# Performance work log

Measured on AMD Instinct MI355X. Metric: run time of the kernel, lower is better.

Reference implementation:

```python
import jax, jax.numpy as jnp
from jax import lax
import numpy as np

IN_SIZE, H_SIZE, OUT_SIZE, SEAS = 48, 128, 48, 24
DILATIONS = (1, 2, 4, 8)  # cells 0-1 = DRNN group 0, cells 2-3 = DRNN group 1


def setup_inputs() -> dict:
    key = jax.random.key(0)
    ks = jax.random.split(key, 16)
    B, T = 256, 512
    inp = {
        'train': jax.random.uniform(ks[0], (B, T), jnp.float32, 0.5, 1.5),
        'val': jax.random.uniform(ks[1], (B, OUT_SIZE), jnp.float32, 0.5, 1.5),
        'test': jax.random.uniform(ks[2], (B, OUT_SIZE), jnp.float32, 0.5, 1.5),
        'init_lev_sm': jnp.array([0.5], jnp.float32),
        'init_seas_sm': jnp.array([0.5], jnp.float32),
        'init_seasonalities': jnp.full((SEAS,), 0.5, jnp.float32),
    }
    cin = [IN_SIZE, H_SIZE, H_SIZE, H_SIZE]
    k = 3
    for i in range(4):
        inp[f'w_ih{i}'] = jax.random.normal(ks[k], (4 * H_SIZE, cin[i]), jnp.float32) * 0.05; k += 1
        inp[f'w_hh{i}'] = jax.random.normal(ks[k], (4 * H_SIZE, H_SIZE), jnp.float32) * 0.05; k += 1
        inp[f'b_ih{i}'] = jnp.zeros((4 * H_SIZE,), jnp.float32)
        inp[f'b_hh{i}'] = jnp.zeros((4 * H_SIZE,), jnp.float32)
    inp['nl_w'] = jax.random.normal(ks[k], (H_SIZE, H_SIZE), jnp.float32) * 0.05; k += 1
    inp['nl_b'] = jnp.zeros((H_SIZE,), jnp.float32)
    inp['sc_w'] = jax.random.normal(ks[k], (OUT_SIZE, H_SIZE), jnp.float32) * 0.05; k += 1
    inp['sc_b'] = jnp.zeros((OUT_SIZE,), jnp.float32)
    return inp


def _lstm(x, w_ih, w_hh, b_ih, b_hh):
    # x: (T, N, C) -> (T, N, H); torch LSTM gate order i, f, g, o
    n, h = x.shape[1], w_hh.shape[1]

    def step(carry, xt):
        hp, cp = carry
        g = xt @ w_ih.T + hp @ w_hh.T + (b_ih + b_hh)
        i, f, gg, o = jnp.split(g, 4, axis=-1)
        c = jax.nn.sigmoid(f) * cp + jax.nn.sigmoid(i) * jnp.tanh(gg)
        hn = jax.nn.sigmoid(o) * jnp.tanh(c)
        return (hn, c), hn

    z = jnp.zeros((n, h), x.dtype)
    _, hs = lax.scan(step, (z, z), x)
    return hs


def _dilated_lstm(x, d, w_ih, w_hh, b_ih, b_hh):
    # DRNN dilation: fold time by d into batch, run cell, unfold
    t, b, c = x.shape
    td = -(-t // d) * d
    xp = jnp.pad(x, ((0, td - t), (0, 0), (0, 0)))
    xd = xp.reshape(td // d, d, b, c).reshape(td // d, d * b, c)
    out = _lstm(xd, w_ih, w_hh, b_ih, b_hh)
    h = out.shape[-1]
    return out.reshape(td // d, d, b, h).reshape(td, b, h)[:t]


def _series_forward(data, cells, nl_w, nl_b, sc_w, sc_b):
    # ResidualDRNN: group 0 (cells 0,1), group 1 (cells 2,3) with residual add
    x = data
    for grp in range(2):
        res = x
        for ci in (2 * grp, 2 * grp + 1):
            x = _dilated_lstm(x, DILATIONS[ci], *cells[ci])
        if grp > 0:
            x = x + res
    x = jnp.tanh(x @ nl_w.T + nl_b)
    return x @ sc_w.T + sc_b


def _esrnn(train, val, init_lev_sm, init_seas_sm, init_seasonalities, cells, nl_w, nl_b, sc_w, sc_b):
    B, T = train.shape
    lev_sm = jax.nn.sigmoid(init_lev_sm[0])
    seas_sm = jax.nn.sigmoid(init_seas_sm[0])
    s0 = jnp.exp(init_seasonalities)  # (SEAS,) shared across series
    lev0 = train[:, 0] / s0[0]  # (B,)
    # rolling buffer: at step i it holds seasonalities[i .. i+SEAS-1]
    buf0 = jnp.broadcast_to(jnp.concatenate([s0[1:], s0[:1]])[:, None], (SEAS, B))

    def step(carry, x_t):
        lev_p, buf = carry
        seas_t = buf[0]
        lev_n = lev_sm * (x_t / seas_t) + (1 - lev_sm) * lev_p
        seas_n = seas_sm * (x_t / lev_n) + (1 - seas_sm) * seas_t
        return (lev_n, jnp.concatenate([buf[1:], seas_n[None]], 0)), (lev_n, seas_n)

    _, (levs_r, seas_r) = lax.scan(step, (lev0, buf0), train[:, 1:].T)
    levs = jnp.concatenate([lev0[None], levs_r], 0).T  # (B, T)
    seas_head = jnp.broadcast_to(jnp.concatenate([s0, s0[:1]])[:, None], (SEAS + 1, B))
    seas = jnp.concatenate([seas_head, seas_r], 0).T  # (B, T+SEAS)
    if OUT_SIZE > SEAS:  # seasonality extension branch
        start = seas.shape[1] - SEAS
        seas = jnp.concatenate([seas, seas[:, start:start + OUT_SIZE - SEAS]], 1)
    W = T - IN_SIZE + 1
    Wo = T - OUT_SIZE - IN_SIZE + 1
    idx_in = jnp.arange(W)[:, None] + jnp.arange(IN_SIZE)[None, :]  # (W, IN)
    win_in = (train[:, idx_in] / seas[:, idx_in] / levs[:, IN_SIZE - 1:, None]).transpose(1, 0, 2)  # (W,B,IN)
    idx_out = jnp.arange(Wo)[:, None] + IN_SIZE + jnp.arange(OUT_SIZE)[None, :]
    win_out = (train[:, idx_out] / seas[:, idx_out] / levs[:, IN_SIZE - 1:IN_SIZE - 1 + Wo, None]).transpose(1, 0, 2)
    network_pred = _series_forward(win_in[:-OUT_SIZE], cells, nl_w, nl_b, sc_w, sc_b)  # (Wo,B,OUT)
    network_act = win_out
    net_out_all = _series_forward(win_in, cells, nl_w, nl_b, sc_w, sc_b)  # (W,B,OUT)
    hold = net_out_all[-1] * seas[:, -OUT_SIZE:] * levs[:, -1:]
    hold_out_pred = hold * (hold > 0).astype(hold.dtype)
    hold_out_act = val  # testing=False path
    hold_out_act_norm = val / seas[:, -OUT_SIZE:] / levs[:, -1:]
    return network_pred, network_act, hold_out_pred, net_out_all, hold_out_act, hold_out_act_norm


def reference(train, val, test, init_lev_sm, init_seas_sm, init_seasonalities,
              w_ih0, w_hh0, b_ih0, b_hh0, w_ih1, w_hh1, b_ih1, b_hh1,
              w_ih2, w_hh2, b_ih2, b_hh2, w_ih3, w_hh3, b_ih3, b_hh3,
              nl_w, nl_b, sc_w, sc_b):
    cells = ((w_ih0, w_hh0, b_ih0, b_hh0), (w_ih1, w_hh1, b_ih1, b_hh1),
             (w_ih2, w_hh2, b_ih2, b_hh2), (w_ih3, w_hh3, b_ih3, b_hh3))
    return _esrnn(train, val, init_lev_sm, init_seas_sm, init_seasonalities,
                  cells, nl_w, nl_b, sc_w, sc_b)
```

## Files before the change

### kernel.cpp

```cpp
#include <hip/hip_runtime.h>
#include <cstdint>
#include <cstddef>

typedef _Float16 half8 __attribute__((ext_vector_type(8)));
typedef _Float16 half4 __attribute__((ext_vector_type(4)));
typedef float floatx4 __attribute__((ext_vector_type(4)));

namespace {
constexpr int kB = 256, kT = 512, kIN = 48, kOUT = 48, kSEAS = 24, kH = 128;
constexpr int kW = kT - kIN + 1;
constexpr int kWO = kT - kOUT - kIN + 1;
constexpr int kNB = kW * kB;
constexpr int kMBLK = kNB / 16;
constexpr float kLOG2E = 1.44269504088896340736f;
}

#if __has_builtin(__builtin_amdgcn_exp2f)
#define FEXP2(x) __builtin_amdgcn_exp2f(x)
#else
#define FEXP2(x) exp2f(x)
#endif
#if __has_builtin(__builtin_amdgcn_rcpf)
#define FRCP(x) __builtin_amdgcn_rcpf(x)
#else
#define FRCP(x) (1.0f / (x))
#endif

__device__ __forceinline__ float fsig(float y) { return FRCP(1.0f + FEXP2(-y)); }
__device__ __forceinline__ float ftanh(float x) { return 2.0f * fsig(2.0f * kLOG2E * x) - 1.0f; }

__global__ void k_transpose(const float* __restrict__ train, float* __restrict__ trainT) {
  int t = blockIdx.x, b = threadIdx.x;
  trainT[t * kB + b] = train[b * kT + t];
}

template <int N>
__device__ __forceinline__ void es_block(int k0, int b, float lev_sm, float omb_l,
                                         float seas_sm, float omb_s, float& lev,
                                         float (&stprev)[kSEAS],
                                         const float* __restrict__ trainT,
                                         float* __restrict__ seas, float* __restrict__ levs,
                                         float* __restrict__ ratio) {
  float x[N], q[N], lv[N];
#pragma unroll
  for (int jj = 0; jj < N; ++jj) x[jj] = trainT[(k0 + jj + 1) * kB + b];
#pragma unroll
  for (int jj = 0; jj < N; ++jj) q[jj] = x[jj] * FRCP(stprev[jj]);
#pragma unroll
  for (int jj = 0; jj < N; ++jj) {
    lev = lev_sm * q[jj] + omb_l * lev;
    lv[jj] = lev;
  }
#pragma unroll
  for (int jj = 0; jj < N; ++jj) {
    float sn = seas_sm * (x[jj] * FRCP(lv[jj])) + omb_s * stprev[jj];
    stprev[jj] = sn;
    seas[(k0 + jj + kSEAS + 1) * kB + b] = sn;
    levs[(k0 + jj + 1) * kB + b] = lv[jj];
    ratio[(k0 + jj + 1) * kB + b] = q[jj];
  }
}

__global__ void k_es(const float* __restrict__ trainT, const float* __restrict__ levp,
                     const float* __restrict__ seasp, const float* __restrict__ inits,
                     float* __restrict__ seas, float* __restrict__ levs,
                     float* __restrict__ ratio) {
  int b = threadIdx.x;
  float lev_sm = fsig(levp[0] * kLOG2E);
  float seas_sm = fsig(seasp[0] * kLOG2E);
  float omb_l = 1.0f - lev_sm, omb_s = 1.0f - seas_sm;
  float stprev[kSEAS];
  float s00 = expf(inits[0]);
#pragma unroll
  for (int s = 0; s < kSEAS; ++s) {
    float v = expf(inits[s]);
    seas[s * kB + b] = v;
    if (s >= 1) stprev[s - 1] = v;
  }
  stprev[kSEAS - 1] = s00;
  seas[kSEAS * kB + b] = s00;
  float lev = trainT[b] * FRCP(s00);
  levs[b] = lev;
  ratio[b] = lev;
#pragma unroll 1
  for (int blk = 0; blk < 21; ++blk)
    es_block<24>(blk * kSEAS, b, lev_sm, omb_l, seas_sm, omb_s, lev, stprev, trainT, seas,
                 levs, ratio);
  es_block<7>(504, b, lev_sm, omb_l, seas_sm, omb_s, lev, stprev, trainT, seas, levs,
              ratio);
  for (int j = 0; j < kOUT - kSEAS; ++j)
    seas[(kT + kSEAS + j) * kB + b] = seas[(kT + j) * kB + b];
}

__global__ void k_win_in(const float* __restrict__ ratio, const float* __restrict__ levs,
                         _Float16* __restrict__ win) {
  int w = blockIdx.x;
  int tid = threadIdx.x;
#pragma unroll
  for (int i = 0; i < 16; ++i) {
    int o = i * 256 + tid;
    int b = o >> 3;
    int j0 = (o & 7) * 8;
    half8 h;
    if (j0 < kIN) {
      float rl = FRCP(levs[(kIN - 1 + w) * kB + b]);
#pragma unroll
      for (int jj = 0; jj < 8; ++jj) {
        int j = j0 + jj;
        float v = (j < kIN) ? ratio[(w + j) * kB + b] * rl : 0.0f;
        h[jj] = (_Float16)v;
      }
    } else {
#pragma unroll
      for (int jj = 0; jj < 8; ++jj) h[jj] = (_Float16)0.0f;
    }
    *(half8*)(win + ((size_t)(w * kB + b)) * 64 + j0) = h;
  }
}

__global__ void k_win_out(const float* __restrict__ ratio, const float* __restrict__ levs,
                          float* __restrict__ out1) {
  int idx = blockIdx.x * 256 + threadIdx.x;
  if (idx >= kWO * kB * (kOUT / 4)) return;
  int row = idx / 12;
  int j0 = (idx - row * 12) * 4;
  int wo = row >> 8;
  int b = row & 255;
  float rl = FRCP(levs[(kIN - 1 + wo) * kB + b]);
  floatx4 v;
#pragma unroll
  for (int jj = 0; jj < 4; ++jj) v[jj] = ratio[(kIN + wo + j0 + jj) * kB + b] * rl;
  *(floatx4*)(out1 + (size_t)row * kOUT + j0) = v;
}

__device__ __forceinline__ void prep_bias_elem(const float* bih, const float* bhh, float* dst,
                                               int c) {
  int ct = c >> 4, n16 = c & 15, g = ct & 3, wv = ct >> 2;
  int row = g * 128 + wv * 16 + n16;
  float sc = (g == 2) ? 2.0f * kLOG2E : kLOG2E;
  dst[c] = (bih[row] + bhh[row]) * sc;
}

__device__ __forceinline__ void prep_frag_elem(const float* Wsrc, _Float16* dst, int KB, int Kreal,
                                               int srcld, int perm, int idx) {
  int jj = idx & 7;
  int lane = (idx >> 3) & 63;
  int kb = (idx >> 9) % KB;
  int ct = idx / (KB * 512);
  int n16 = lane & 15;
  int k = kb * 32 + ((lane >> 4) << 3) + jj;
  int row;
  float sc;
  if (perm) {
    int g = ct & 3, wv = ct >> 2;
    row = g * 128 + wv * 16 + n16;
    sc = (g == 2) ? 2.0f * kLOG2E : kLOG2E;
  } else {
    row = ct * 16 + n16;
    sc = 1.0f;
  }
  float v = (k < Kreal) ? Wsrc[row * srcld + k] * sc : 0.0f;
  dst[idx] = (_Float16)v;
}

struct PrepArgs {
  const float* bih[4];
  const float* bhh[4];
  float* biasp[4];
  const float* wih[4];
  _Float16* wihf[4];
  const float* whh[4];
  _Float16* whhf[4];
  const float* nlw;
  _Float16* nlf;
  const float* scw;
  _Float16* scf;
};

__global__ void k_prep_all(PrepArgs a) {
  int seg = blockIdx.y;
  int idx = blockIdx.x * 256 + threadIdx.x;
  if (seg < 4) {
    if (idx < 512) prep_bias_elem(a.bih[seg], a.bhh[seg], a.biasp[seg], idx);
  } else if (seg == 4) {
    if (idx < 32 * 2 * 512) prep_frag_elem(a.wih[0], a.wihf[0], 2, 48, 48, 1, idx);
  } else if (seg < 8) {
    int c = seg - 4;
    if (idx < 32 * 4 * 512) prep_frag_elem(a.wih[c], a.wihf[c], 4, 128, 128, 1, idx);
  } else if (seg < 12) {
    int c = seg - 8;
    if (idx < 32 * 4 * 512) prep_frag_elem(a.whh[c], a.whhf[c], 4, 128, 128, 1, idx);
  } else if (seg == 12) {
    if (idx < 8 * 4 * 512) prep_frag_elem(a.nlw, a.nlf, 4, 128, 128, 0, idx);
  } else {
    if (idx < 3 * 4 * 512) prep_frag_elem(a.scw, a.scf, 4, 128, 128, 0, idx);
  }
}

__global__ void k_zero_prog(int* prog) {
  prog[threadIdx.x] = 0;
}

template <int NT, int KB, int MODE>
__global__ __launch_bounds__(512) void k_gemm(const _Float16* __restrict__ A,
                                              const _Float16* __restrict__ A2, int Khalfs,
                                              const _Float16* __restrict__ Bfr,
                                              const float* __restrict__ bias,
                                              _Float16* __restrict__ outh,
                                              float* __restrict__ outf,
                                              float* __restrict__ outf2) {
  __shared__ _Float16 bsh[NT * KB * 512];
  int tid = threadIdx.x;
  {
    const uint4* src = (const uint4*)Bfr;
    uint4* dst = (uint4*)bsh;
    for (int i = tid; i < NT * KB * 64; i += 512) dst[i] = src[i];
  }
  __syncthreads();
  int wv = tid >> 6, lane = tid & 63;
  int mblk = blockIdx.x * 8 + wv;
  if (mblk >= kMBLK) return;
  int m = lane & 15, kq = lane >> 4;
  const _Float16* arow = A + (size_t)(mblk * 16 + m) * Khalfs + kq * 8;
  half8 af[KB];
#pragma unroll
  for (int kb = 0; kb < KB; ++kb) af[kb] = *(const half8*)(arow + kb * 32);
  if constexpr (MODE == 1) {
    const _Float16* arow2 = A2 + (size_t)(mblk * 16 + m) * Khalfs + kq * 8;
#pragma unroll
    for (int kb = 0; kb < KB; ++kb) {
      half8 a2 = *(const half8*)(arow2 + kb * 32);
      af[kb] += a2;
    }
  }
#pragma unroll
  for (int t0 = 0; t0 < NT; t0 += 2) {
    float b0 = bias[t0 * 16 + m];
    floatx4 acc0 = {b0, b0, b0, b0};
    floatx4 acc1 = {0.f, 0.f, 0.f, 0.f};
    if (t0 + 1 < NT) {
      float b1 = bias[(t0 + 1) * 16 + m];
      acc1 = (floatx4){b1, b1, b1, b1};
    }
#pragma unroll
    for (int kb = 0; kb < KB; ++kb) {
      half8 bf0 = *(const half8*)(&bsh[((t0 * KB + kb) * 64 + lane) * 8]);
      acc0 = __builtin_amdgcn_mfma_f32_16x16x32_f16(af[kb], bf0, acc0, 0, 0, 0);
      if (t0 + 1 < NT) {
        half8 bf1 = *(const half8*)(&bsh[(((t0 + 1) * KB + kb) * 64 + lane) * 8]);
        acc1 = __builtin_amdgcn_mfma_f32_16x16x32_f16(af[kb], bf1, acc1, 0, 0, 0);
      }
    }
    if constexpr (MODE == 1) {
#pragma unroll
      for (int r = 0; r < 4; ++r) {
        int row = mblk * 16 + kq * 4 + r;
        outh[(size_t)row * kH + t0 * 16 + m] = (_Float16)ftanh(acc0[r]);
        if (t0 + 1 < NT) outh[(size_t)row * kH + (t0 + 1) * 16 + m] = (_Float16)ftanh(acc1[r]);
      }
    } else {
#pragma unroll
      for (int r = 0; r < 4; ++r) {
        int row = mblk * 16 + kq * 4 + r;
        float v0 = acc0[r];
        outf[(size_t)row * kOUT + t0 * 16 + m] = v0;
        if (row < kWO * kB) outf2[(size_t)row * kOUT + t0 * 16 + m] = v0;
        if (t0 + 1 < NT) {
          float v1 = acc1[r];
          outf[(size_t)row * kOUT + (t0 + 1) * 16 + m] = v1;
          if (row < kWO * kB) outf2[(size_t)row * kOUT + (t0 + 1) * 16 + m] = v1;
        }
      }
    }
  }
}

struct FArgs {
  const _Float16* win;
  const _Float16* wihf[4];
  const _Float16* whhf[4];
  const float* biasp[4];
  _Float16* H[4];
  int* prog;
};

__device__ __forceinline__ void wait_prog(int* p, int need, int& fenced, int* obs_sh) {
  if (need <= fenced) return;
  if (threadIdx.x == 0) {
    int v;
    while ((v = __hip_atomic_load(p, __ATOMIC_RELAXED, __HIP_MEMORY_SCOPE_AGENT)) < need)
      __builtin_amdgcn_s_sleep(16);
    *obs_sh = v;
  }
  __syncthreads();
  int v = *obs_sh;
  __builtin_amdgcn_fence(__ATOMIC_ACQUIRE, "agent");
  fenced = v;
}

template <int KXB, bool POLL, bool REL>
__device__ __forceinline__ void floop(const _Float16* __restrict__ Xsrc,
                                      const _Float16* __restrict__ wihp,
                                      const _Float16* __restrict__ whhp,
                                      const float* __restrict__ bp, _Float16* __restrict__ Hout,
                                      int* progIn, int sprev, int* progOut, int d, int kd, int ib,
                                      _Float16 (*hbuf)[2048], int* obs_sh) {
  int tid = threadIdx.x;
  int wv = tid >> 6, lane = tid & 63, m = lane & 15, kq = lane >> 4;
  half8 wxf[4][KXB], whf[4][4];
#pragma unroll
  for (int g = 0; g < 4; ++g) {
#pragma unroll
    for (int kb = 0; kb < KXB; ++kb)
      wxf[g][kb] = *(const half8*)(wihp + ((((wv * 4 + g) * KXB + kb) * 64 + lane) * 8));
#pragma unroll
    for (int kb = 0; kb < 4; ++kb)
      whf[g][kb] = *(const half8*)(whhp + ((((wv * 4 + g) * 4 + kb) * 64 + lane) * 8));
  }
  float bg[4];
#pragma unroll
  for (int g = 0; g < 4; ++g) bg[g] = bp[(wv * 4 + g) * 16 + m];
  float cc[4] = {0.f, 0.f, 0.f, 0.f};
  int nsteps = (kW - kd + d - 1) / d;
  const int xstride = KXB * 32;
  int fenced = 0;
  if (POLL) wait_prog(progIn + (kd & ((1 << sprev) - 1)), (kd >> sprev) + 1, fenced, obs_sh);
  half8 hxc[KXB], hxn[KXB];
  {
    const _Float16* xrow = Xsrc + (size_t)(kd * kB + ib * 16 + m) * xstride + kq * 8;
#pragma unroll
    for (int kb = 0; kb < KXB; ++kb) hxc[kb] = *(const half8*)(xrow + kb * 32);
  }
  for (int j = 0; j < nsteps; ++j) {
    int ph = j & 1;
    int wtn = (j + 1) * d + kd;
    bool havenext = (j + 1 < nsteps);
    if (POLL && havenext)
      wait_prog(progIn + (wtn & ((1 << sprev) - 1)), (wtn >> sprev) + 1, fenced, obs_sh);
    floatx4 acc[4];
#pragma unroll
    for (int g = 0; g < 4; ++g) acc[g] = (floatx4){bg[g], bg[g], bg[g], bg[g]};
    if (havenext) {
      const _Float16* xrow = Xsrc + (size_t)(wtn * kB + ib * 16 + m) * xstride + kq * 8;
#pragma unroll
      for (int kb = 0; kb < KXB; ++kb) hxn[kb] = *(const half8*)(xrow + kb * 32);
    }
#pragma unroll
    for (int kb = 0; kb < KXB; ++kb)
#pragma unroll
      for (int g = 0; g < 4; ++g)
        acc[g] = __builtin_amdgcn_mfma_f32_16x16x32_f16(hxc[kb], wxf[g][kb], acc[g], 0, 0, 0);
    if (j > 0) {
#pragma unroll
      for (int kb = 0; kb < 4; ++kb) {
        int gran = (kb * 4 + kq) ^ m;
        half8 a = *(const half8*)(&hbuf[ph ^ 1][m * 128 + gran * 8]);
#pragma unroll
        for (int g = 0; g < 4; ++g)
          acc[g] = __builtin_amdgcn_mfma_f32_16x16x32_f16(a, whf[g][kb], acc[g], 0, 0, 0);
      }
    }
    _Float16 hv[4];
#pragma unroll
    for (int r = 0; r < 4; ++r) {
      float iv = fsig(acc[0][r]);
      float fv = fsig(acc[1][r]);
      float g2 = fsig(acc[2][r]);
      float ov = fsig(acc[3][r]);
      cc[r] = fv * cc[r] + iv * (2.0f * g2 - 1.0f);
      float tc = 2.0f * fsig(cc[r] * (2.0f * kLOG2E)) - 1.0f;
      hv[r] = (_Float16)(ov * tc);
      int brow = kq * 4 + r;
      int hu = wv * 16 + m;
      int gran = (hu >> 3) ^ brow;
      hbuf[ph][brow * 128 + gran * 8 + (hu & 7)] = hv[r];
    }
    __syncthreads();
    {
      int hu = wv * 16 + m;
      size_t rb = (size_t)((j * d + kd) * kB + ib * 16 + kq * 4);
#pragma unroll
      for (int r = 0; r < 4; ++r) Hout[(rb + r) * kH + hu] = hv[r];
    }
    if (REL && (((j & 7) == 7) || (j + 1 == nsteps))) {
      __syncthreads();
      if (tid == 0)
        __hip_atomic_store(progOut, j + 1, __ATOMIC_RELEASE, __HIP_MEMORY_SCOPE_AGENT);
    }
#pragma unroll
    for (int kb = 0; kb < KXB; ++kb) hxc[kb] = hxn[kb];
  }
}

__global__ __launch_bounds__(512) void k_fused(FArgs a) {
  __shared__ _Float16 hbuf[2][2048];
  __shared__ int obs_sh;
  int w = blockIdx.x;
  int cell, d, kd, ib;
  if (w < 16) {
    cell = 0; d = 1; kd = 0; ib = w;
  } else if (w < 48) {
    cell = 1; d = 2; kd = (w - 16) >> 4; ib = (w - 16) & 15;
  } else if (w < 112) {
    cell = 2; d = 4; kd = (w - 48) >> 4; ib = (w - 48) & 15;
  } else {
    cell = 3; d = 8; kd = (w - 112) >> 4; ib = (w - 112) & 15;
  }
  const _Float16* Xsrc = (cell == 0) ? a.win : a.H[cell - 1];
  _Float16* Hout = a.H[cell];
  int* progOut = a.prog + (cell * 16 + ib) * 4 + kd;
  int* progIn = (cell > 0) ? a.prog + ((cell - 1) * 16 + ib) * 4 : nullptr;
  int sprev = (cell == 2) ? 1 : ((cell == 3) ? 2 : 0);
  if (cell == 0)
    floop<2, false, true>(Xsrc, a.wihf[0], a.whhf[0], a.biasp[0], Hout, nullptr, 0, progOut, d,
                          kd, ib, hbuf, &obs_sh);
  else if (cell < 3)
    floop<4, true, true>(Xsrc, a.wihf[cell], a.whhf[cell], a.biasp[cell], Hout, progIn, sprev,
                         progOut, d, kd, ib, hbuf, &obs_sh);
  else
    floop<4, true, false>(Xsrc, a.wihf[3], a.whhf[3], a.biasp[3], Hout, progIn, sprev, progOut,
                          d, kd, ib, hbuf, &obs_sh);
}

__global__ void k_tail(const float* __restrict__ out3, const float* __restrict__ val,
                       const float* __restrict__ seas, const float* __restrict__ levs,
                       float* __restrict__ out2, float* __restrict__ out4,
                       float* __restrict__ out5) {
  int idx = blockIdx.x * 256 + threadIdx.x;
  int b = idx / kOUT, j = idx % kOUT;
  float s = seas[(kT + j) * kB + b];
  float L = levs[(kT - 1) * kB + b];
  float net = out3[(size_t)(kW - 1) * kB * kOUT + idx];
  float hp = net * s * L;
  out2[idx] = hp > 0.0f ? hp : 0.0f;
  float v = val[idx];
  out4[idx] = v;
  out5[idx] = v / s / L;
}

extern "C" void kernel_launch(void* const* d_in, const int* in_sizes, int n_in, void* d_out,
                              int out_size, void* d_ws, size_t ws_size, hipStream_t stream) {
  const float* train = (const float*)d_in[0];
  const float* val = (const float*)d_in[1];
  const float* levp = (const float*)d_in[3];
  const float* seasp = (const float*)d_in[4];
  const float* inits = (const float*)d_in[5];
  const float* w_ih[4] = {(const float*)d_in[6], (const float*)d_in[10], (const float*)d_in[14],
                          (const float*)d_in[18]};
  const float* w_hh[4] = {(const float*)d_in[7], (const float*)d_in[11], (const float*)d_in[15],
                          (const float*)d_in[19]};
  const float* b_ih[4] = {(const float*)d_in[8], (const float*)d_in[12], (const float*)d_in[16],
                          (const float*)d_in[20]};
  const float* b_hh[4] = {(const float*)d_in[9], (const float*)d_in[13], (const float*)d_in[17],
                          (const float*)d_in[21]};
  const float* nl_w = (const float*)d_in[22];
  const float* nl_b = (const float*)d_in[23];
  const float* sc_w = (const float*)d_in[24];
  const float* sc_b = (const float*)d_in[25];

  char* wsb = (char*)d_ws;
  size_t off = 0;
  auto alloc = [&](size_t bytes) -> void* {
    void* p = wsb + off;
    off = (off + bytes + 255) & ~(size_t)255;
    return p;
  };
  float* trainT = (float*)alloc((size_t)kT * kB * 4);
  float* seas = (float*)alloc((size_t)560 * kB * 4);
  float* levs = (float*)alloc((size_t)kT * kB * 4);
  float* ratio = (float*)alloc((size_t)kT * kB * 4);
  _Float16* win = (_Float16*)alloc((size_t)kNB * 64 * 2);
  _Float16* Hc[4];
  for (int c = 0; c < 4; ++c) Hc[c] = (_Float16*)alloc((size_t)kNB * kH * 2);
  _Float16* U = (_Float16*)alloc((size_t)kNB * kH * 2);
  float* biasp[4];
  for (int c = 0; c < 4; ++c) biasp[c] = (float*)alloc(512 * 4);
  _Float16* wihf[4];
  wihf[0] = (_Float16*)alloc((size_t)32 * 2 * 512 * 2);
  for (int c = 1; c < 4; ++c) wihf[c] = (_Float16*)alloc((size_t)32 * 4 * 512 * 2);
  _Float16* whhf[4];
  for (int c = 0; c < 4; ++c) whhf[c] = (_Float16*)alloc((size_t)32 * 4 * 512 * 2);
  _Float16* nlf = (_Float16*)alloc((size_t)8 * 4 * 512 * 2);
  _Float16* scf = (_Float16*)alloc((size_t)3 * 4 * 512 * 2);
  int* prog = (int*)alloc(256 * 4);

  float* out0 = (float*)d_out;
  float* out1 = out0 + (size_t)kWO * kB * kOUT;
  float* out2 = out1 + (size_t)kWO * kB * kOUT;
  float* out3 = out2 + (size_t)kB * kOUT;
  float* out4 = out3 + (size_t)kW * kB * kOUT;
  float* out5 = out4 + (size_t)kB * kOUT;

  k_transpose<<<kT, kB, 0, stream>>>(train, trainT);
  k_es<<<1, kB, 0, stream>>>(trainT, levp, seasp, inits, seas, levs, ratio);
  k_win_in<<<kW, kB, 0, stream>>>(ratio, levs, win);
  k_win_out<<<(kWO * kB * 12 + 255) / 256, 256, 0, stream>>>(ratio, levs, out1);

  PrepArgs pa;
  for (int c = 0; c < 4; ++c) {
    pa.bih[c] = b_ih[c]; pa.bhh[c] = b_hh[c]; pa.biasp[c] = biasp[c];
    pa.wih[c] = w_ih[c]; pa.wihf[c] = wihf[c];
    pa.whh[c] = w_hh[c]; pa.whhf[c] = whhf[c];
  }
  pa.nlw = nl_w; pa.nlf = nlf; pa.scw = sc_w; pa.scf = scf;
  k_prep_all<<<dim3(256, 14), 256, 0, stream>>>(pa);
  k_zero_prog<<<1, 256, 0, stream>>>(prog);

  FArgs fa;
  fa.win = win;
  for (int c = 0; c < 4; ++c) {
    fa.wihf[c] = wihf[c]; fa.whhf[c] = whhf[c]; fa.biasp[c] = biasp[c]; fa.H[c] = Hc[c];
  }
  fa.prog = prog;
  void* kp[1] = {(void*)&fa};
  hipLaunchCooperativeKernel((void*)k_fused, dim3(240), dim3(512), kp, 0, stream);

  const int GG = kMBLK / 8;
  k_gemm<8, 4, 1><<<GG, 512, 0, stream>>>(Hc[3], Hc[1], 128, nlf, nl_b, U, nullptr, nullptr);
  k_gemm<3, 4, 2><<<GG, 512, 0, stream>>>(U, nullptr, 128, scf, sc_b, nullptr, out3, out0);
  k_tail<<<48, 256, 0, stream>>>(out3, val, seas, levs, out2, out4, out5);
}
```

Before: 687.8 us.

## Overlap output head with LSTM wavefront inside fused kernel and merge prep kernels

The separate nonlinear and scale GEMM kernels are folded into the cooperative kernel as 16 extra blocks. These blocks poll the progress counters of cells 3 and 1 and compute the head per timestep while the recurrence is still running. Cell 3 now publishes progress every 2 steps, which adds more release barriers to that cell. The transpose kernel is removed (k_es reads train rows directly), the two window kernels are merged into one, and progress zeroing moves into the prep kernel, which cuts the number of launches.

New measurement: 1.548 ms. +125.1%, slower.

```diff
diff --git a/kernel.cpp b/kernel.cpp
--- a/kernel.cpp
+++ b/kernel.cpp
@@ -13,6 +13,7 @@
 constexpr int kNB = kW * kB;
 constexpr int kMBLK = kNB / 16;
 constexpr float kLOG2E = 1.44269504088896340736f;
+constexpr int kWOBLK = (kWO * kB * 12 + 255) / 256;
 }
 
 #if __has_builtin(__builtin_amdgcn_exp2f)
@@ -26,24 +27,20 @@
 #define FRCP(x) (1.0f / (x))
 #endif
 
+#define LGKM_BARRIER() asm volatile("s_waitcnt lgkmcnt(0)\n\ts_barrier" ::: "memory")
+
 __device__ __forceinline__ float fsig(float y) { return FRCP(1.0f + FEXP2(-y)); }
 __device__ __forceinline__ float ftanh(float x) { return 2.0f * fsig(2.0f * kLOG2E * x) - 1.0f; }
-
-__global__ void k_transpose(const float* __restrict__ train, float* __restrict__ trainT) {
-  int t = blockIdx.x, b = threadIdx.x;
-  trainT[t * kB + b] = train[b * kT + t];
-}
 
 template <int N>
 __device__ __forceinline__ void es_block(int k0, int b, float lev_sm, float omb_l,
                                          float seas_sm, float omb_s, float& lev,
-                                         float (&stprev)[kSEAS],
-                                         const float* __restrict__ trainT,
+                                         float (&stprev)[kSEAS], const float* __restrict__ trow,
                                          float* __restrict__ seas, float* __restrict__ levs,
                                          float* __restrict__ ratio) {
   float x[N], q[N], lv[N];
 #pragma unroll
-  for (int jj = 0; jj < N; ++jj) x[jj] = trainT[(k0 + jj + 1) * kB + b];
+  for (int jj = 0; jj < N; ++jj) x[jj] = trow[k0 + jj + 1];
 #pragma unroll
   for (int jj = 0; jj < N; ++jj) q[jj] = x[jj] * FRCP(stprev[jj]);
 #pragma unroll
@@ -61,11 +58,12 @@
   }
 }
 
-__global__ void k_es(const float* __restrict__ trainT, const float* __restrict__ levp,
+__global__ void k_es(const float* __restrict__ train, const float* __restrict__ levp,
                      const float* __restrict__ seasp, const float* __restrict__ inits,
                      float* __restrict__ seas, float* __restrict__ levs,
                      float* __restrict__ ratio) {
   int b = threadIdx.x;
+  const float* trow = train + (size_t)b * kT;
   float lev_sm = fsig(levp[0] * kLOG2E);
   float seas_sm = fsig(seasp[0] * kLOG2E);
   float omb_l = 1.0f - lev_sm, omb_s = 1.0f - seas_sm;
@@ -79,58 +77,56 @@
   }
   stprev[kSEAS - 1] = s00;
   seas[kSEAS * kB + b] = s00;
-  float lev = trainT[b] * FRCP(s00);
+  float lev = trow[0] * FRCP(s00);
   levs[b] = lev;
   ratio[b] = lev;
 #pragma unroll 1
   for (int blk = 0; blk < 21; ++blk)
-    es_block<24>(blk * kSEAS, b, lev_sm, omb_l, seas_sm, omb_s, lev, stprev, trainT, seas,
-                 levs, ratio);
-  es_block<7>(504, b, lev_sm, omb_l, seas_sm, omb_s, lev, stprev, trainT, seas, levs,
-              ratio);
+    es_block<24>(blk * kSEAS, b, lev_sm, omb_l, seas_sm, omb_s, lev, stprev, trow, seas, levs,
+                 ratio);
+  es_block<7>(504, b, lev_sm, omb_l, seas_sm, omb_s, lev, stprev, trow, seas, levs, ratio);
   for (int j = 0; j < kOUT - kSEAS; ++j)
     seas[(kT + kSEAS + j) * kB + b] = seas[(kT + j) * kB + b];
 }
 
-__global__ void k_win_in(const float* __restrict__ ratio, const float* __restrict__ levs,
-                         _Float16* __restrict__ win) {
+__global__ void k_win(const float* __restrict__ ratio, const float* __restrict__ levs,
+                      _Float16* __restrict__ win, float* __restrict__ out1) {
   int w = blockIdx.x;
   int tid = threadIdx.x;
-#pragma unroll
-  for (int i = 0; i < 16; ++i) {
-    int o = i * 256 + tid;
-    int b = o >> 3;
-    int j0 = (o & 7) * 8;
-    half8 h;
-    if (j0 < kIN) {
-      float rl = FRCP(levs[(kIN - 1 + w) * kB + b]);
-#pragma unroll
-      for (int jj = 0; jj < 8; ++jj) {
-        int j = j0 + jj;
-        float v = (j < kIN) ? ratio[(w + j) * kB + b] * rl : 0.0f;
-        h[jj] = (_Float16)v;
-      }
-    } else {
-#pragma unroll
-      for (int jj = 0; jj < 8; ++jj) h[jj] = (_Float16)0.0f;
-    }
-    *(half8*)(win + ((size_t)(w * kB + b)) * 64 + j0) = h;
-  }
-}
-
-__global__ void k_win_out(const float* __restrict__ ratio, const float* __restrict__ levs,
-                          float* __restrict__ out1) {
-  int idx = blockIdx.x * 256 + threadIdx.x;
-  if (idx >= kWO * kB * (kOUT / 4)) return;
-  int row = idx / 12;
-  int j0 = (idx - row * 12) * 4;
-  int wo = row >> 8;
-  int b = row & 255;
-  float rl = FRCP(levs[(kIN - 1 + wo) * kB + b]);
-  floatx4 v;
-#pragma unroll
-  for (int jj = 0; jj < 4; ++jj) v[jj] = ratio[(kIN + wo + j0 + jj) * kB + b] * rl;
-  *(floatx4*)(out1 + (size_t)row * kOUT + j0) = v;
+  if (w < kW) {
+#pragma unroll
+    for (int i = 0; i < 16; ++i) {
+      int o = i * 256 + tid;
+      int b = o >> 3;
+      int j0 = (o & 7) * 8;
+      half8 h;
+      if (j0 < kIN) {
+        float rl = FRCP(levs[(kIN - 1 + w) * kB + b]);
+#pragma unroll
+        for (int jj = 0; jj < 8; ++jj) {
+          int j = j0 + jj;
+          float v = (j < kIN) ? ratio[(w + j) * kB + b] * rl : 0.0f;
+          h[jj] = (_Float16)v;
+        }
+      } else {
+#pragma unroll
+        for (int jj = 0; jj < 8; ++jj) h[jj] = (_Float16)0.0f;
+      }
+      *(half8*)(win + ((size_t)(w * kB + b)) * 64 + j0) = h;
+    }
+  } else {
+    int idx = (w - kW) * 256 + tid;
+    if (idx >= kWO * kB * 12) return;
+    int row = idx / 12;
+    int j0 = (idx - row * 12) * 4;
+    int wo = row >> 8;
+    int b = row & 255;
+    float rl = FRCP(levs[(kIN - 1 + wo) * kB + b]);
+    floatx4 v;
+#pragma unroll
+    for (int jj = 0; jj < 4; ++jj) v[jj] = ratio[(kIN + wo + j0 + jj) * kB + b] * rl;
+    *(floatx4*)(out1 + (size_t)row * kOUT + j0) = v;
+  }
 }
 
 __device__ __forceinline__ void prep_bias_elem(const float* bih, const float* bhh, float* dst,
@@ -175,6 +171,7 @@
   _Float16* nlf;
   const float* scw;
   _Float16* scf;
+  int* prog;
 };
 
 __global__ void k_prep_all(PrepArgs a) {
@@ -192,86 +189,10 @@
     if (idx < 32 * 4 * 512) prep_frag_elem(a.whh[c], a.whhf[c], 4, 128, 128, 1, idx);
   } else if (seg == 12) {
     if (idx < 8 * 4 * 512) prep_frag_elem(a.nlw, a.nlf, 4, 128, 128, 0, idx);
+  } else if (seg == 13) {
+    if (idx < 3 * 4 * 512) prep_frag_elem(a.scw, a.scf, 4, 128, 128, 0, idx);
   } else {
-    if (idx < 3 * 4 * 512) prep_frag_elem(a.scw, a.scf, 4, 128, 128, 0, idx);
-  }
-}
-
-__global__ void k_zero_prog(int* prog) {
-  prog[threadIdx.x] = 0;
-}
-
-template <int NT, int KB, int MODE>
-__global__ __launch_bounds__(512) void k_gemm(const _Float16* __restrict__ A,
-                                              const _Float16* __restrict__ A2, int Khalfs,
-                                              const _Float16* __restrict__ Bfr,
-                                              const float* __restrict__ bias,
-                                              _Float16* __restrict__ outh,
-                                              float* __restrict__ outf,
-                                              float* __restrict__ outf2) {
-  __shared__ _Float16 bsh[NT * KB * 512];
-  int tid = threadIdx.x;
-  {
-    const uint4* src = (const uint4*)Bfr;
-    uint4* dst = (uint4*)bsh;
-    for (int i = tid; i < NT * KB * 64; i += 512) dst[i] = src[i];
-  }
-  __syncthreads();
-  int wv = tid >> 6, lane = tid & 63;
-  int mblk = blockIdx.x * 8 + wv;
-  if (mblk >= kMBLK) return;
-  int m = lane & 15, kq = lane >> 4;
-  const _Float16* arow = A + (size_t)(mblk * 16 + m) * Khalfs + kq * 8;
-  half8 af[KB];
-#pragma unroll
-  for (int kb = 0; kb < KB; ++kb) af[kb] = *(const half8*)(arow + kb * 32);
-  if constexpr (MODE == 1) {
-    const _Float16* arow2 = A2 + (size_t)(mblk * 16 + m) * Khalfs + kq * 8;
-#pragma unroll
-    for (int kb = 0; kb < KB; ++kb) {
-      half8 a2 = *(const half8*)(arow2 + kb * 32);
-      af[kb] += a2;
-    }
-  }
-#pragma unroll
-  for (int t0 = 0; t0 < NT; t0 += 2) {
-    float b0 = bias[t0 * 16 + m];
-    floatx4 acc0 = {b0, b0, b0, b0};
-    floatx4 acc1 = {0.f, 0.f, 0.f, 0.f};
-    if (t0 + 1 < NT) {
-      float b1 = bias[(t0 + 1) * 16 + m];
-      acc1 = (floatx4){b1, b1, b1, b1};
-    }
-#pragma unroll
-    for (int kb = 0; kb < KB; ++kb) {
-      half8 bf0 = *(const half8*)(&bsh[((t0 * KB + kb) * 64 + lane) * 8]);
-      acc0 = __builtin_amdgcn_mfma_f32_16x16x32_f16(af[kb], bf0, acc0, 0, 0, 0);
-      if (t0 + 1 < NT) {
-        half8 bf1 = *(const half8*)(&bsh[(((t0 + 1) * KB + kb) * 64 + lane) * 8]);
-        acc1 = __builtin_amdgcn_mfma_f32_16x16x32_f16(af[kb], bf1, acc1, 0, 0, 0);
-      }
-    }
-    if constexpr (MODE == 1) {
-#pragma unroll
-      for (int r = 0; r < 4; ++r) {
-        int row = mblk * 16 + kq * 4 + r;
-        outh[(size_t)row * kH + t0 * 16 + m] = (_Float16)ftanh(acc0[r]);
-        if (t0 + 1 < NT) outh[(size_t)row * kH + (t0 + 1) * 16 + m] = (_Float16)ftanh(acc1[r]);
-      }
-    } else {
-#pragma unroll
-      for (int r = 0; r < 4; ++r) {
-        int row = mblk * 16 + kq * 4 + r;
-        float v0 = acc0[r];
-        outf[(size_t)row * kOUT + t0 * 16 + m] = v0;
-        if (row < kWO * kB) outf2[(size_t)row * kOUT + t0 * 16 + m] = v0;
-        if (t0 + 1 < NT) {
-          float v1 = acc1[r];
-          outf[(size_t)row * kOUT + (t0 + 1) * 16 + m] = v1;
-          if (row < kWO * kB) outf2[(size_t)row * kOUT + (t0 + 1) * 16 + m] = v1;
-        }
-      }
-    }
+    if (idx < 320) a.prog[idx] = 0;
   }
 }
 
@@ -282,6 +203,12 @@
   const float* biasp[4];
   _Float16* H[4];
   int* prog;
+  const _Float16* nlf;
+  const _Float16* scf;
+  const float* nlb;
+  const float* scb;
+  float* out3;
+  float* out0;
 };
 
 __device__ __forceinline__ void wait_prog(int* p, int need, int& fenced, int* obs_sh) {
@@ -298,7 +225,7 @@
   fenced = v;
 }
 
-template <int KXB, bool POLL, bool REL>
+template <int KXB, bool POLL, bool REL, int RELMASK>
 __device__ __forceinline__ void floop(const _Float16* __restrict__ Xsrc,
                                       const _Float16* __restrict__ wihp,
                                       const _Float16* __restrict__ whhp,
@@ -382,13 +309,98 @@
 #pragma unroll
       for (int r = 0; r < 4; ++r) Hout[(rb + r) * kH + hu] = hv[r];
     }
-    if (REL && (((j & 7) == 7) || (j + 1 == nsteps))) {
+    if (REL && (((j & RELMASK) == RELMASK) || (j + 1 == nsteps))) {
       __syncthreads();
       if (tid == 0)
         __hip_atomic_store(progOut, j + 1, __ATOMIC_RELEASE, __HIP_MEMORY_SCOPE_AGENT);
     }
 #pragma unroll
     for (int kb = 0; kb < KXB; ++kb) hxc[kb] = hxn[kb];
+  }
+}
+
+__device__ void tail_loop(const FArgs& a, int ib, _Float16 (*hbuf)[2048]) {
+  int tid = threadIdx.x;
+  int wv = tid >> 6, lane = tid & 63, m = lane & 15, kq = lane >> 4;
+  half8 nf[4], sf[4];
+  int cts = (wv < 3) ? wv : 0;
+#pragma unroll
+  for (int kb = 0; kb < 4; ++kb) {
+    nf[kb] = *(const half8*)(a.nlf + ((size_t)((wv * 4 + kb) * 64 + lane)) * 8);
+    sf[kb] = *(const half8*)(a.scf + ((size_t)((cts * 4 + kb) * 64 + lane)) * 8);
+  }
+  float nb = a.nlb[wv * 16 + m];
+  float sb = (wv < 3) ? a.scb[wv * 16 + m] : 0.0f;
+  int* prog3 = a.prog + 192 + ib * 8;
+  int* prog1 = a.prog + (16 + ib) * 4;
+  const _Float16* H3 = a.H[3];
+  const _Float16* H1 = a.H[1];
+  for (int t0 = 0; t0 < kW; t0 += 8) {
+    int tend = (t0 + 8 < kW) ? t0 + 8 : kW;
+    if (tid == 0) {
+      int need3 = (t0 >> 3) + 1;
+      for (int kd = 0; kd < 8; ++kd) {
+        if (t0 + kd >= tend) break;
+        while (__hip_atomic_load(prog3 + kd, __ATOMIC_RELAXED, __HIP_MEMORY_SCOPE_AGENT) < need3)
+          __builtin_amdgcn_s_sleep(16);
+      }
+      for (int kd = 0; kd < 2; ++kd) {
+        int tmaxk = tend - 1;
+        if ((tmaxk & 1) != kd) --tmaxk;
+        if (tmaxk < t0) continue;
+        int need1 = (tmaxk >> 1) + 1;
+        while (__hip_atomic_load(prog1 + kd, __ATOMIC_RELAXED, __HIP_MEMORY_SCOPE_AGENT) < need1)
+          __builtin_amdgcn_s_sleep(16);
+      }
+    }
+    __syncthreads();
+    __builtin_amdgcn_fence(__ATOMIC_ACQUIRE, "agent");
+#pragma unroll 1
+    for (int t = t0; t < tend; ++t) {
+      int ph = t & 1;
+      const _Float16* r3 = H3 + (size_t)(t * kB + ib * 16 + m) * kH + kq * 8;
+      const _Float16* r1 = H1 + (size_t)(t * kB + ib * 16 + m) * kH + kq * 8;
+      half8 af[4];
+#pragma unroll
+      for (int kb = 0; kb < 4; ++kb) {
+        half8 v3 = *(const half8*)(r3 + kb * 32);
+        half8 v1 = *(const half8*)(r1 + kb * 32);
+        af[kb] = v3 + v1;
+      }
+      floatx4 acc = {nb, nb, nb, nb};
+#pragma unroll
+      for (int kb = 0; kb < 4; ++kb)
+        acc = __builtin_amdgcn_mfma_f32_16x16x32_f16(af[kb], nf[kb], acc, 0, 0, 0);
+#pragma unroll
+      for (int r = 0; r < 4; ++r) {
+        _Float16 uv = (_Float16)ftanh(acc[r]);
+        int brow = kq * 4 + r;
+        int hu = wv * 16 + m;
+        int gran = (hu >> 3) ^ brow;
+        hbuf[ph][brow * 128 + gran * 8 + (hu & 7)] = uv;
+      }
+      LGKM_BARRIER();
+      if (wv < 3) {
+        half8 uf[4];
+#pragma unroll
+        for (int kb = 0; kb < 4; ++kb) {
+          int gran = (kb * 4 + kq) ^ m;
+          uf[kb] = *(const half8*)(&hbuf[ph][m * 128 + gran * 8]);
+        }
+        floatx4 a2 = {sb, sb, sb, sb};
+#pragma unroll
+        for (int kb = 0; kb < 4; ++kb)
+          a2 = __builtin_amdgcn_mfma_f32_16x16x32_f16(uf[kb], sf[kb], a2, 0, 0, 0);
+        size_t row = (size_t)t * kB + ib * 16 + kq * 4;
+        bool dup = (t < kWO);
+#pragma unroll
+        for (int r = 0; r < 4; ++r) {
+          float v = a2[r];
+          a.out3[(row + r) * kOUT + wv * 16 + m] = v;
+          if (dup) a.out0[(row + r) * kOUT + wv * 16 + m] = v;
+        }
+      }
+    }
   }
 }
 
@@ -396,6 +408,10 @@
   __shared__ _Float16 hbuf[2][2048];
   __shared__ int obs_sh;
   int w = blockIdx.x;
+  if (w >= 240) {
+    tail_loop(a, w - 240, hbuf);
+    return;
+  }
   int cell, d, kd, ib;
   if (w < 16) {
     cell = 0; d = 1; kd = 0; ib = w;
@@ -408,18 +424,18 @@
   }
   const _Float16* Xsrc = (cell == 0) ? a.win : a.H[cell - 1];
   _Float16* Hout = a.H[cell];
-  int* progOut = a.prog + (cell * 16 + ib) * 4 + kd;
+  int* progOut = (cell == 3) ? a.prog + 192 + ib * 8 + kd : a.prog + (cell * 16 + ib) * 4 + kd;
   int* progIn = (cell > 0) ? a.prog + ((cell - 1) * 16 + ib) * 4 : nullptr;
   int sprev = (cell == 2) ? 1 : ((cell == 3) ? 2 : 0);
   if (cell == 0)
-    floop<2, false, true>(Xsrc, a.wihf[0], a.whhf[0], a.biasp[0], Hout, nullptr, 0, progOut, d,
-                          kd, ib, hbuf, &obs_sh);
+    floop<2, false, true, 7>(Xsrc, a.wihf[0], a.whhf[0], a.biasp[0], Hout, nullptr, 0, progOut,
+                             d, kd, ib, hbuf, &obs_sh);
   else if (cell < 3)
-    floop<4, true, true>(Xsrc, a.wihf[cell], a.whhf[cell], a.biasp[cell], Hout, progIn, sprev,
-                         progOut, d, kd, ib, hbuf, &obs_sh);
+    floop<4, true, true, 7>(Xsrc, a.wihf[cell], a.whhf[cell], a.biasp[cell], Hout, progIn,
+                            sprev, progOut, d, kd, ib, hbuf, &obs_sh);
   else
-    floop<4, true, false>(Xsrc, a.wihf[3], a.whhf[3], a.biasp[3], Hout, progIn, sprev, progOut,
-                          d, kd, ib, hbuf, &obs_sh);
+    floop<4, true, true, 1>(Xsrc, a.wihf[3], a.whhf[3], a.biasp[3], Hout, progIn, sprev,
+                            progOut, d, kd, ib, hbuf, &obs_sh);
 }
 
 __global__ void k_tail(const float* __restrict__ out3, const float* __restrict__ val,
@@ -465,14 +481,12 @@
     off = (off + bytes + 255) & ~(size_t)255;
     return p;
   };
-  float* trainT = (float*)alloc((size_t)kT * kB * 4);
   float* seas = (float*)alloc((size_t)560 * kB * 4);
   float* levs = (float*)alloc((size_t)kT * kB * 4);
   float* ratio = (float*)alloc((size_t)kT * kB * 4);
   _Float16* win = (_Float16*)alloc((size_t)kNB * 64 * 2);
   _Float16* Hc[4];
   for (int c = 0; c < 4; ++c) Hc[c] = (_Float16*)alloc((size_t)kNB * kH * 2);
-  _Float16* U = (_Float16*)alloc((size_t)kNB * kH * 2);
   float* biasp[4];
   for (int c = 0; c < 4; ++c) biasp[c] = (float*)alloc(512 * 4);
   _Float16* wihf[4];
@@ -482,7 +496,7 @@
   for (int c = 0; c < 4; ++c) whhf[c] = (_Float16*)alloc((size_t)32 * 4 * 512 * 2);
   _Float16* nlf = (_Float16*)alloc((size_t)8 * 4 * 512 * 2);
   _Float16* scf = (_Float16*)alloc((size_t)3 * 4 * 512 * 2);
-  int* prog = (int*)alloc(256 * 4);
+  int* prog = (int*)alloc(320 * 4);
 
   float* out0 = (float*)d_out;
   float* out1 = out0 + (size_t)kWO * kB * kOUT;
@@ -491,10 +505,8 @@
   float* out4 = out3 + (size_t)kW * kB * kOUT;
   float* out5 = out4 + (size_t)kB * kOUT;
 
-  k_transpose<<<kT, kB, 0, stream>>>(train, trainT);
-  k_es<<<1, kB, 0, stream>>>(trainT, levp, seasp, inits, seas, levs, ratio);
-  k_win_in<<<kW, kB, 0, stream>>>(ratio, levs, win);
-  k_win_out<<<(kWO * kB * 12 + 255) / 256, 256, 0, stream>>>(ratio, levs, out1);
+  k_es<<<1, kB, 0, stream>>>(train, levp, seasp, inits, seas, levs, ratio);
+  k_win<<<kW + kWOBLK, kB, 0, stream>>>(ratio, levs, win, out1);
 
   PrepArgs pa;
   for (int c = 0; c < 4; ++c) {
@@ -502,9 +514,8 @@
     pa.wih[c] = w_ih[c]; pa.wihf[c] = wihf[c];
     pa.whh[c] = w_hh[c]; pa.whhf[c] = whhf[c];
   }
-  pa.nlw = nl_w; pa.nlf = nlf; pa.scw = sc_w; pa.scf = scf;
-  k_prep_all<<<dim3(256, 14), 256, 0, stream>>>(pa);
-  k_zero_prog<<<1, 256, 0, stream>>>(prog);
+  pa.nlw = nl_w; pa.nlf = nlf; pa.scw = sc_w; pa.scf = scf; pa.prog = prog;
+  k_prep_all<<<dim3(256, 15), 256, 0, stream>>>(pa);
 
   FArgs fa;
   fa.win = win;
@@ -512,11 +523,10 @@
     fa.wihf[c] = wihf[c]; fa.whhf[c] = whhf[c]; fa.biasp[c] = biasp[c]; fa.H[c] = Hc[c];
   }
   fa.prog = prog;
+  fa.nlf = nlf; fa.scf = scf; fa.nlb = nl_b; fa.scb = sc_b;
+  fa.out3 = out3; fa.out0 = out0;
   void* kp[1] = {(void*)&fa};
-  hipLaunchCooperativeKernel((void*)k_fused, dim3(240), dim3(512), kp, 0, stream);
-
-  const int GG = kMBLK / 8;
-  k_gemm<8, 4, 1><<<GG, 512, 0, stream>>>(Hc[3], Hc[1], 128, nlf, nl_b, U, nullptr, nullptr);
-  k_gemm<3, 4, 2><<<GG, 512, 0, stream>>>(U, nullptr, 128, scf, sc_b, nullptr, out3, out0);
+  hipLaunchCooperativeKernel((void*)k_fused, dim3(256), dim3(512), kp, 0, stream);
+
   k_tail<<<48, 256, 0, stream>>>(out3, val, seas, levs, out2, out4, out5);
 }
```
